# Kernel optimization log

Hardware: AMD Instinct MI355X
Metric: run time of the kernel (lower is better)

Reference implementation:

```python
import jax, jax.numpy as jnp
import numpy as np

DEPTH = 3
WIDTH = 512
WIDTH_SUB = 256
B = 64
L = 512
EPS = 1e-5
C_IN = 2 * WIDTH_SUB  # == WIDTH here, so per-depth params stack uniformly


def setup_inputs() -> dict:
    key = jax.random.key(0)
    ks = jax.random.split(key, 4)
    s = 1.0 / np.sqrt(C_IN).astype(np.float32)
    P_matrix = jax.random.normal(ks[0], (B, C_IN, L), jnp.float32)
    Wq = jax.random.normal(ks[1], (DEPTH, WIDTH, C_IN), jnp.float32) * s
    Wk = jax.random.normal(ks[2], (DEPTH, WIDTH, C_IN), jnp.float32) * s
    Wv = jax.random.normal(ks[3], (DEPTH, WIDTH, C_IN), jnp.float32) * s
    zeros = jnp.zeros((DEPTH, WIDTH), jnp.float32)
    ones = jnp.ones((DEPTH, WIDTH), jnp.float32)
    return {
        "P_matrix": P_matrix,
        "Wq": Wq, "bq": zeros, "gq": ones, "betaq": zeros,
        "Wk": Wk, "bk": zeros, "gk": ones, "betak": zeros,
        "Wv": Wv, "bv": zeros, "gv": ones, "betav": zeros,
    }


def _ncl_linear(x, W, b, gamma, beta):
    # x: [B, C, L]; Linear over channel dim, then BatchNorm1d (training stats) + ReLU
    y = jnp.einsum('bcl,oc->bol', x, W) + b[None, :, None]  # [B, O, L]
    mean = y.mean(axis=(0, 2), keepdims=True)
    var = y.var(axis=(0, 2), keepdims=True)  # biased, as torch BN uses for normalization
    y = (y - mean) * jax.lax.rsqrt(var + EPS) * gamma[None, :, None] + beta[None, :, None]
    return jax.nn.relu(y)


def reference(P_matrix, Wq, bq, gq, betaq, Wk, bk, gk, betak, Wv, bv, gv, betav):
    x = P_matrix
    for i in range(DEPTH):
        Q = _ncl_linear(x, Wq[i], bq[i], gq[i], betaq[i])  # [B, W, L]
        K = _ncl_linear(x, Wk[i], bk[i], gk[i], betak[i])
        V = _ncl_linear(x, Wv[i], bv[i], gv[i], betav[i])
        w = jnp.einsum('bcl,bdl->bcd', Q, K)  # [B, W, W], unscaled
        # nn.Softmax() with dim=None on a 3D tensor -> dim=0 in torch
        a = jax.nn.softmax(w, axis=0)
        x = jnp.einsum('bcd,bdl->bcl', a, V)  # [B, W, L]
    return x
```

## Files before the change

### kernel.cpp

```cpp
#include <hip/hip_runtime.h>
#include <hip/hip_fp8.h>
#include <stdint.h>

typedef __bf16 bf16_t;
typedef bf16_t bf16x8 __attribute__((ext_vector_type(8)));
typedef bf16_t bf16x4 __attribute__((ext_vector_type(4)));
typedef float  f32x4  __attribute__((ext_vector_type(4)));

#define MFMA_BF16(a,b,c) __builtin_amdgcn_mfma_f32_16x16x32_bf16(a,b,c,0,0,0)

__device__ __forceinline__ void load_lds16(const bf16_t* g, bf16_t* l) {
  __builtin_amdgcn_global_load_lds((const __attribute__((address_space(1))) void*)g,
                                   (__attribute__((address_space(3))) void*)l,
                                   16, 0, 0);
}

__device__ __forceinline__ float fp8_to_f(uint8_t b) {
  return (float)__builtin_bit_cast(__hip_fp8_e4m3, b);
}
__device__ __forceinline__ uint8_t f_to_fp8(float f) {
  return __builtin_bit_cast(uint8_t, __hip_fp8_e4m3(f));
}
__device__ __forceinline__ uint8_t fp8s_enc(float r) { return f_to_fp8(r * 256.f); }
__device__ __forceinline__ float   fp8s_dec(uint8_t b) { return fp8_to_f(b) * (1.f/256.f); }

__device__ __forceinline__ bf16x8 dec8(uint64_t v) {
  bf16x8 o;
#pragma unroll
  for (int j = 0; j < 8; ++j) o[j] = (bf16_t)fp8s_dec((uint8_t)(v >> (8*j)));
  return o;
}

__global__ __launch_bounds__(256) void cast_w_kern(const float* __restrict__ wq,
    const float* __restrict__ wk, const float* __restrict__ wv,
    bf16_t* __restrict__ whi, bf16_t* __restrict__ wlo) {
  const int i = blockIdx.x * 256 + threadIdx.x;
  const int idx = i * 4;
  const int p = idx / 786432;
  const int r = idx - p * 786432;
  const float* s = (p == 0 ? wq : (p == 1 ? wk : wv));
  float4 v = *(const float4*)(s + r);
  float f[4] = {v.x, v.y, v.z, v.w};
  bf16x4 hi, lo;
#pragma unroll
  for (int j = 0; j < 4; ++j) {
    bf16_t h = (bf16_t)f[j];
    hi[j] = h;
    lo[j] = (bf16_t)(f[j] - (float)h);
  }
  const size_t o = (size_t)p * 786432 + r;
  *(bf16x4*)(whi + o) = hi;
  *(bf16x4*)(wlo + o) = lo;
}

__global__ __launch_bounds__(256) void transpose_split_in_kern(
    const float* __restrict__ P, bf16_t* __restrict__ xh, uint8_t* __restrict__ xl) {
  __shared__ float t[32][33];
  const int bz = blockIdx.x >> 8;
  const int ti = blockIdx.x & 255;
  const int tc = (ti >> 4) * 32;
  const int tl = (ti & 15) * 32;
  const float* Pb = P + (size_t)bz * 262144;
  bf16_t* xb = xh + (size_t)bz * 262144;
  uint8_t* lb = xl + (size_t)bz * 262144;
  const int tx = threadIdx.x & 31, ty = threadIdx.x >> 5;
#pragma unroll
  for (int k = 0; k < 4; ++k)
    t[ty*4+k][tx] = Pb[(size_t)(tc + ty*4 + k)*512 + tl + tx];
  __syncthreads();
#pragma unroll
  for (int k = 0; k < 4; ++k) {
    const float f = t[tx][ty*4+k];
    const bf16_t h = (bf16_t)f;
    const size_t o = (size_t)(tl + ty*4 + k)*512 + tc + tx;
    xb[o] = h;
    lb[o] = fp8s_enc(f - (float)h);
  }
}

__global__ __launch_bounds__(256) void gemm_qkv_kern(
    const bf16_t* __restrict__ Whi, const bf16_t* __restrict__ Wlo,
    const bf16_t* __restrict__ xh, const uint8_t* __restrict__ xl,
    const float* __restrict__ bq, const float* __restrict__ bk,
    const float* __restrict__ bv, int depth,
    bf16_t* __restrict__ Qh, uint8_t* __restrict__ Ql,
    bf16_t* __restrict__ Kh, uint8_t* __restrict__ Kl,
    bf16_t* __restrict__ Yvh, bf16_t* __restrict__ Yvl,
    float* __restrict__ bsum, float* __restrict__ bsum2) {
  __shared__ __align__(16) bf16_t Ah[4096], Al[4096], Bh[4096], Bl[4096];
  const int blk = blockIdx.x;
  const int t  = blk & 15;
  const int pb = blk >> 4;
  const int b  = pb & 63, p = pb >> 6;
  const int row0 = (t >> 2) * 128, col0 = (t & 3) * 128;
  const size_t woff = (size_t)p * 786432 + (size_t)depth * 262144;
  const bf16_t* A_hi = Whi + woff;
  const bf16_t* A_lo = Wlo + woff;
  const bf16_t* B_hi = xh + (size_t)b * 262144;
  const uint8_t* B_lo = xl + (size_t)b * 262144;
  const int tid = threadIdx.x, lane = tid & 63, wid = tid >> 6;
  const int wm = wid >> 1, wn = wid & 1;
  const int sr = tid >> 2, scs = (tid & 3) * 8;
  const int frow = lane & 15, fk = (lane >> 4) * 8;
  f32x4 acc[4][4] = {};
  bf16_t* lah = Ah + wid * 512;
  bf16_t* lal = Al + wid * 512;
  bf16_t* lbh = Bh + wid * 512;
  const bf16_t* gah = A_hi + (size_t)(row0 + sr) * 512 + scs;
  const bf16_t* gal = A_lo + (size_t)(row0 + sr) * 512 + scs;
  const bf16_t* gbh = B_hi + (size_t)(col0 + sr) * 512 + scs;
  const uint8_t* gbl = B_lo + (size_t)(col0 + sr) * 512 + scs;
  for (int ks = 0; ks < 16; ++ks) {
    const int k0 = ks * 32;
    load_lds16(gah + k0, lah); load_lds16(gah + 32768 + k0, lah + 2048);
    load_lds16(gal + k0, lal); load_lds16(gal + 32768 + k0, lal + 2048);
    load_lds16(gbh + k0, lbh); load_lds16(gbh + 32768 + k0, lbh + 2048);
    {
      const uint64_t r0 = *(const uint64_t*)(gbl + k0);
      const uint64_t r1 = *(const uint64_t*)(gbl + 32768 + k0);
      *(bf16x8*)(Bl + sr*32 + scs)        = dec8(r0);
      *(bf16x8*)(Bl + 2048 + sr*32 + scs) = dec8(r1);
    }
    __syncthreads();
    bf16x8 ah[4], al[4], bh[4], bl[4];
#pragma unroll
    for (int i = 0; i < 4; ++i) {
      const int ai = (wm*64 + i*16 + frow)*32 + fk;
      const int bi = (wn*64 + i*16 + frow)*32 + fk;
      ah[i] = *(const bf16x8*)(Ah + ai);
      al[i] = *(const bf16x8*)(Al + ai);
      bh[i] = *(const bf16x8*)(Bh + bi);
      bl[i] = *(const bf16x8*)(Bl + bi);
    }
#pragma unroll
    for (int i = 0; i < 4; ++i)
#pragma unroll
      for (int j = 0; j < 4; ++j) {
        acc[i][j] = MFMA_BF16(ah[i], bh[j], acc[i][j]);
        acc[i][j] = MFMA_BF16(al[i], bh[j], acc[i][j]);
        acc[i][j] = MFMA_BF16(ah[i], bl[j], acc[i][j]);
      }
    __syncthreads();
  }
  const float* bias = (p == 0 ? bq : (p == 1 ? bk : bv)) + depth * 512;
  if (p < 2) {
    bf16_t* Oh = (p == 0 ? Qh : Kh) + (size_t)b * 262144;
    uint8_t* Ol = (p == 0 ? Ql : Kl) + (size_t)b * 262144;
#pragma unroll
    for (int i = 0; i < 4; ++i)
#pragma unroll
      for (int r = 0; r < 4; ++r) {
        const int rr = row0 + wm*64 + i*16 + (lane >> 4)*4 + r;
        const float bb = bias[rr];
        float s = 0.f, ss = 0.f;
#pragma unroll
        for (int j = 0; j < 4; ++j) {
          const int cc = col0 + wn*64 + j*16 + (lane & 15);
          const float y = acc[i][j][r] + bb;
          s += y; ss += y * y;
          const bf16_t h = (bf16_t)y;
          Oh[(size_t)rr * 512 + cc] = h;
          Ol[(size_t)rr * 512 + cc] = fp8s_enc(y - (float)h);
        }
#pragma unroll
        for (int m = 1; m < 16; m <<= 1) {
          s  += __shfl_xor(s, m);
          ss += __shfl_xor(ss, m);
        }
        if ((lane & 15) == 0) {
          atomicAdd(&bsum[p * 512 + rr], s);
          atomicAdd(&bsum2[p * 512 + rr], ss);
        }
      }
  } else {
    bf16_t* Ovh = Yvh + (size_t)b * 262144;
    bf16_t* Ovl = Yvl + (size_t)b * 262144;
#pragma unroll
    for (int i = 0; i < 4; ++i)
#pragma unroll
      for (int r = 0; r < 4; ++r) {
        const int rr = row0 + wm*64 + i*16 + (lane >> 4)*4 + r;
        const float bb = bias[rr];
        float s = 0.f, ss = 0.f;
#pragma unroll
        for (int j = 0; j < 4; ++j) {
          const int cc = col0 + wn*64 + j*16 + (lane & 15);
          const float y = acc[i][j][r] + bb;
          s += y; ss += y * y;
          const bf16_t h = (bf16_t)y;
          Ovh[(size_t)rr * 512 + cc] = h;
          Ovl[(size_t)rr * 512 + cc] = (bf16_t)(y - (float)h);
        }
#pragma unroll
        for (int m = 1; m < 16; m <<= 1) {
          s  += __shfl_xor(s, m);
          ss += __shfl_xor(ss, m);
        }
        if ((lane & 15) == 0) {
          atomicAdd(&bsum[1024 + rr], s);
          atomicAdd(&bsum2[1024 + rr], ss);
        }
      }
  }
}

__global__ __launch_bounds__(256) void bn_finalize_kern(
    float* __restrict__ bsum, float* __restrict__ bsum2,
    const float* __restrict__ gq, const float* __restrict__ gk, const float* __restrict__ gv,
    const float* __restrict__ betaq, const float* __restrict__ betak, const float* __restrict__ betav,
    int depth, float* __restrict__ scale, float* __restrict__ shift) {
  const int po = blockIdx.x * 256 + threadIdx.x;
  const int p = po >> 9, o = po & 511;
  const float mean = bsum[po] * (1.f / 32768.f);
  float var = bsum2[po] * (1.f / 32768.f) - mean * mean;
  var = fmaxf(var, 0.f);
  const float* gp = (p == 0 ? gq : (p == 1 ? gk : gv));
  const float* bp = (p == 0 ? betaq : (p == 1 ? betak : betav));
  const float gamma = gp[depth * 512 + o];
  const float beta  = bp[depth * 512 + o];
  const float sc = gamma * rsqrtf(var + 1e-5f);
  scale[po] = sc;
  shift[po] = beta - mean * sc;
  bsum[po] = 0.f;
  bsum2[po] = 0.f;
}

__global__ __launch_bounds__(256) void norm_qk_kern(
    bf16_t* __restrict__ Qh, uint8_t* __restrict__ Ql,
    bf16_t* __restrict__ Kh, uint8_t* __restrict__ Kl,
    const float* __restrict__ scale, const float* __restrict__ shift) {
  const size_t i = ((size_t)blockIdx.x * 256 + threadIdx.x) * 4;
  const int p = (int)(i >> 24);
  const size_t j = i & 0xFFFFFF;
  const int o = (int)(j >> 9) & 511;
  const int po = p * 512 + o;
  const float sc = scale[po], sh = shift[po];
  bf16_t* H = (p == 0 ? Qh : Kh) + j;
  uint8_t* L = (p == 0 ? Ql : Kl) + j;
  bf16x4 hv = *(bf16x4*)H;
  uint32_t lv = *(uint32_t*)L;
  bf16x4 ho;
  uint32_t lo_out = 0;
#pragma unroll
  for (int k = 0; k < 4; ++k) {
    const float y = (float)hv[k] + fp8s_dec((uint8_t)(lv >> (8*k)));
    const float q = fmaxf(y * sc + sh, 0.f);
    const bf16_t h = (bf16_t)q;
    ho[k] = h;
    lo_out |= (uint32_t)fp8s_enc(q - (float)h) << (8*k);
  }
  *(bf16x4*)H = ho;
  *(uint32_t*)L = lo_out;
}

__global__ __launch_bounds__(256) void norm_v_t_kern(
    const bf16_t* __restrict__ Yvh, const bf16_t* __restrict__ Yvl,
    const float* __restrict__ scale, const float* __restrict__ shift,
    bf16_t* __restrict__ VTh, uint8_t* __restrict__ VTl) {
  __shared__ float t[32][33];
  const int bz = blockIdx.x >> 8;
  const int ti = blockIdx.x & 255;
  const int td = (ti >> 4) * 32;
  const int tl = (ti & 15) * 32;
  const size_t boff = (size_t)bz * 262144;
  const int tx = threadIdx.x & 31, ty = threadIdx.x >> 5;
#pragma unroll
  for (int k = 0; k < 4; ++k) {
    const int dd = td + ty*4 + k;
    const float sc = scale[1024 + dd], sh = shift[1024 + dd];
    const size_t o = boff + (size_t)dd * 512 + tl + tx;
    const float f = (float)Yvh[o] + (float)Yvl[o];
    t[ty*4+k][tx] = fmaxf(f * sc + sh, 0.f);
  }
  __syncthreads();
#pragma unroll
  for (int k = 0; k < 4; ++k) {
    const float v = t[tx][ty*4+k];
    const bf16_t h = (bf16_t)v;
    const size_t o = boff + (size_t)(tl + ty*4 + k)*512 + td + tx;
    VTh[o] = h;
    VTl[o] = fp8s_enc(v - (float)h);
  }
}

__global__ __launch_bounds__(256) void gemm_w_kern(
    const bf16_t* __restrict__ Qh, const uint8_t* __restrict__ Ql,
    const bf16_t* __restrict__ Kh, const uint8_t* __restrict__ Kl,
    float* __restrict__ w) {
  __shared__ __align__(16) bf16_t Ah[4096], Al[4096], Bh[4096], Bl[4096];
  const int blk = blockIdx.x;
  const int t = blk & 15;
  const int b = blk >> 4;
  const int row0 = (t >> 2) * 128, col0 = (t & 3) * 128;
  const bf16_t* A_hi = Qh + (size_t)b * 262144;
  const uint8_t* A_lo = Ql + (size_t)b * 262144;
  const bf16_t* B_hi = Kh + (size_t)b * 262144;
  const uint8_t* B_lo = Kl + (size_t)b * 262144;
  const int tid = threadIdx.x, lane = tid & 63, wid = tid >> 6;
  const int wm = wid >> 1, wn = wid & 1;
  const int sr = tid >> 2, scs = (tid & 3) * 8;
  const int frow = lane & 15, fk = (lane >> 4) * 8;
  f32x4 acc[4][4] = {};
  bf16_t* lah = Ah + wid * 512;
  bf16_t* lbh = Bh + wid * 512;
  const bf16_t* gah = A_hi + (size_t)(row0 + sr) * 512 + scs;
  const bf16_t* gbh = B_hi + (size_t)(col0 + sr) * 512 + scs;
  const uint8_t* gal = A_lo + (size_t)(row0 + sr) * 512 + scs;
  const uint8_t* gbl = B_lo + (size_t)(col0 + sr) * 512 + scs;
  for (int ks = 0; ks < 16; ++ks) {
    const int k0 = ks * 32;
    load_lds16(gah + k0, lah); load_lds16(gah + 32768 + k0, lah + 2048);
    load_lds16(gbh + k0, lbh); load_lds16(gbh + 32768 + k0, lbh + 2048);
    {
      const uint64_t ra0 = *(const uint64_t*)(gal + k0);
      const uint64_t ra1 = *(const uint64_t*)(gal + 32768 + k0);
      const uint64_t rb0 = *(const uint64_t*)(gbl + k0);
      const uint64_t rb1 = *(const uint64_t*)(gbl + 32768 + k0);
      *(bf16x8*)(Al + sr*32 + scs)        = dec8(ra0);
      *(bf16x8*)(Al + 2048 + sr*32 + scs) = dec8(ra1);
      *(bf16x8*)(Bl + sr*32 + scs)        = dec8(rb0);
      *(bf16x8*)(Bl + 2048 + sr*32 + scs) = dec8(rb1);
    }
    __syncthreads();
    bf16x8 ah[4], al[4], bh[4], bl[4];
#pragma unroll
    for (int i = 0; i < 4; ++i) {
      const int ai = (wm*64 + i*16 + frow)*32 + fk;
      const int bi = (wn*64 + i*16 + frow)*32 + fk;
      ah[i] = *(const bf16x8*)(Ah + ai);
      al[i] = *(const bf16x8*)(Al + ai);
      bh[i] = *(const bf16x8*)(Bh + bi);
      bl[i] = *(const bf16x8*)(Bl + bi);
    }
#pragma unroll
    for (int i = 0; i < 4; ++i)
#pragma unroll
      for (int j = 0; j < 4; ++j) {
        acc[i][j] = MFMA_BF16(ah[i], bh[j], acc[i][j]);
        acc[i][j] = MFMA_BF16(al[i], bh[j], acc[i][j]);
        acc[i][j] = MFMA_BF16(ah[i], bl[j], acc[i][j]);
      }
    __syncthreads();
  }
  float* wb = w + (size_t)b * 262144;
#pragma unroll
  for (int i = 0; i < 4; ++i)
#pragma unroll
    for (int j = 0; j < 4; ++j)
#pragma unroll
      for (int r = 0; r < 4; ++r) {
        const int rr = row0 + wm*64 + i*16 + (lane >> 4)*4 + r;
        const int cc = col0 + wn*64 + j*16 + (lane & 15);
        wb[(size_t)rr * 512 + cc] = acc[i][j][r];
      }
}

__global__ __launch_bounds__(256) void softmax_kern(float* __restrict__ w) {
  const int idx = blockIdx.x * 256 + threadIdx.x;
  float v[64];
#pragma unroll
  for (int b = 0; b < 64; ++b) v[b] = w[idx + (size_t)b * 262144];
  float m = v[0];
#pragma unroll
  for (int b = 1; b < 64; ++b) m = fmaxf(m, v[b]);
  float s = 0.f;
#pragma unroll
  for (int b = 0; b < 64; ++b) { v[b] = __expf(v[b] - m); s += v[b]; }
  const float inv = 1.f / s;
#pragma unroll
  for (int b = 0; b < 64; ++b) w[idx + (size_t)b * 262144] = v[b] * inv;
}

__global__ __launch_bounds__(256) void gemm_x_kern(
    const bf16_t* __restrict__ VTh, const uint8_t* __restrict__ VTl,
    const float* __restrict__ a,
    bf16_t* __restrict__ xh, uint8_t* __restrict__ xl) {
  __shared__ __align__(16) bf16_t Ah[4096], Al[4096], Bh[4096], Bl[4096];
  const int blk = blockIdx.x;
  const int t = blk & 15;
  const int b = blk >> 4;
  const int row0 = (t >> 2) * 128, col0 = (t & 3) * 128;
  const bf16_t* Ahg = VTh + (size_t)b * 262144;
  const uint8_t* Alg = VTl + (size_t)b * 262144;
  const float*   Bg  = a   + (size_t)b * 262144;
  const int tid = threadIdx.x, lane = tid & 63, wid = tid >> 6;
  const int wm = wid >> 1, wn = wid & 1;
  const int sr = tid >> 2, scs = (tid & 3) * 8;
  const int frow = lane & 15, fk = (lane >> 4) * 8;
  f32x4 acc[4][4] = {};
  bf16_t* lah = Ah + wid * 512;
  const bf16_t* gah = Ahg + (size_t)(row0 + sr) * 512 + scs;
  const uint8_t* gal = Alg + (size_t)(row0 + sr) * 512 + scs;
  for (int ks = 0; ks < 16; ++ks) {
    const int k0 = ks * 32;
    load_lds16(gah + k0, lah); load_lds16(gah + 32768 + k0, lah + 2048);
    {
      const uint64_t r0 = *(const uint64_t*)(gal + k0);
      const uint64_t r1 = *(const uint64_t*)(gal + 32768 + k0);
      *(bf16x8*)(Al + sr*32 + scs)        = dec8(r0);
      *(bf16x8*)(Al + 2048 + sr*32 + scs) = dec8(r1);
    }
    {
#pragma unroll
      for (int p = 0; p < 4; ++p) {
        const int idx = p * 256 + tid;
        const int br = idx >> 3;
        const int cs = (idx & 7) * 4;
        float4 v4 = *(const float4*)(Bg + (size_t)(col0 + br) * 512 + k0 + cs);
        float f[4] = {v4.x, v4.y, v4.z, v4.w};
        bf16x4 hv, lv;
#pragma unroll
        for (int j = 0; j < 4; ++j) {
          bf16_t h = (bf16_t)f[j];
          hv[j] = h;
          lv[j] = (bf16_t)(f[j] - (float)h);
        }
        *(bf16x4*)(Bh + br*32 + cs) = hv;
        *(bf16x4*)(Bl + br*32 + cs) = lv;
      }
    }
    __syncthreads();
    bf16x8 ah[4], al[4], bh[4], bl[4];
#pragma unroll
    for (int i = 0; i < 4; ++i) {
      const int ai = (wm*64 + i*16 + frow)*32 + fk;
      const int bi = (wn*64 + i*16 + frow)*32 + fk;
      ah[i] = *(const bf16x8*)(Ah + ai);
      al[i] = *(const bf16x8*)(Al + ai);
      bh[i] = *(const bf16x8*)(Bh + bi);
      bl[i] = *(const bf16x8*)(Bl + bi);
    }
#pragma unroll
    for (int i = 0; i < 4; ++i)
#pragma unroll
      for (int j = 0; j < 4; ++j) {
        acc[i][j] = MFMA_BF16(ah[i], bh[j], acc[i][j]);
        acc[i][j] = MFMA_BF16(al[i], bh[j], acc[i][j]);
        acc[i][j] = MFMA_BF16(ah[i], bl[j], acc[i][j]);
      }
    __syncthreads();
  }
  bf16_t* xb = xh + (size_t)b * 262144;
  uint8_t* lb8 = xl + (size_t)b * 262144;
#pragma unroll
  for (int i = 0; i < 4; ++i)
#pragma unroll
    for (int j = 0; j < 4; ++j)
#pragma unroll
      for (int r = 0; r < 4; ++r) {
        const int rr = row0 + wm*64 + i*16 + (lane >> 4)*4 + r;
        const int cc = col0 + wn*64 + j*16 + (lane & 15);
        const float y = acc[i][j][r];
        const bf16_t h = (bf16_t)y;
        xb[(size_t)rr * 512 + cc] = h;
        lb8[(size_t)rr * 512 + cc] = fp8s_enc(y - (float)h);
      }
}

__global__ __launch_bounds__(256) void out_transpose_kern(
    const bf16_t* __restrict__ xh, const uint8_t* __restrict__ xl,
    float* __restrict__ out) {
  __shared__ float t[32][33];
  const int bz = blockIdx.x >> 8;
  const int ti = blockIdx.x & 255;
  const int tl = (ti >> 4) * 32;
  const int tc = (ti & 15) * 32;
  const bf16_t* xb = xh + (size_t)bz * 262144;
  const uint8_t* lb = xl + (size_t)bz * 262144;
  float* ob = out + (size_t)bz * 262144;
  const int tx = threadIdx.x & 31, ty = threadIdx.x >> 5;
#pragma unroll
  for (int k = 0; k < 4; ++k) {
    const size_t o = (size_t)(tl + ty*4 + k)*512 + tc + tx;
    t[ty*4+k][tx] = (float)xb[o] + fp8s_dec(lb[o]);
  }
  __syncthreads();
#pragma unroll
  for (int k = 0; k < 4; ++k)
    ob[(size_t)(tc + ty*4 + k)*512 + tl + tx] = t[tx][ty*4+k];
}

extern "C" void kernel_launch(void* const* d_in, const int* in_sizes, int n_in,
                              void* d_out, int out_size, void* d_ws, size_t ws_size,
                              hipStream_t stream) {
  const float* P     = (const float*)d_in[0];
  const float* Wq    = (const float*)d_in[1];
  const float* bq    = (const float*)d_in[2];
  const float* gq    = (const float*)d_in[3];
  const float* betaq = (const float*)d_in[4];
  const float* Wk    = (const float*)d_in[5];
  const float* bk    = (const float*)d_in[6];
  const float* gk    = (const float*)d_in[7];
  const float* betak = (const float*)d_in[8];
  const float* Wv    = (const float*)d_in[9];
  const float* bv    = (const float*)d_in[10];
  const float* gv    = (const float*)d_in[11];
  const float* betav = (const float*)d_in[12];

  char* ws = (char*)d_ws;
  size_t off = 0;
  auto alloc = [&](size_t bytes) -> char* {
    char* p = ws + off;
    off += (bytes + 255) & ~(size_t)255;
    return p;
  };
  bf16_t*  Sh[3]; uint8_t* Sl[3];
  for (int i = 0; i < 3; ++i) {
    Sh[i] = (bf16_t*) alloc(33554432);
    Sl[i] = (uint8_t*)alloc(16777216);
  }
  char* E = alloc(67108864);
  float*  w   = (float*)E;
  bf16_t* Yvh = (bf16_t*)E;
  bf16_t* Yvl = (bf16_t*)(E + 33554432);
  bf16_t* Whi = (bf16_t*)alloc(4718592);
  bf16_t* Wlo = (bf16_t*)alloc(4718592);
  float* scale = (float*)alloc(6144);
  float* shift = (float*)alloc(6144);
  float* bsum  = (float*)alloc(6144);
  float* bsum2 = (float*)alloc(6144);

  hipMemsetAsync(bsum, 0, 12288, stream);
  cast_w_kern<<<2304, 256, 0, stream>>>(Wq, Wk, Wv, Whi, Wlo);
  transpose_split_in_kern<<<16384, 256, 0, stream>>>(P, Sh[0], Sl[0]);
  for (int d = 0; d < 3; ++d) {
    const int xi = (d == 1) ? 1 : 0;
    const int qi = (d == 1) ? 0 : 1;
    const int ki = 2;
    const int ni = (d == 2) ? 2 : qi;
    gemm_qkv_kern<<<3072, 256, 0, stream>>>(Whi, Wlo, Sh[xi], Sl[xi],
        bq, bk, bv, d, Sh[qi], Sl[qi], Sh[ki], Sl[ki], Yvh, Yvl, bsum, bsum2);
    bn_finalize_kern<<<6, 256, 0, stream>>>(bsum, bsum2, gq, gk, gv,
        betaq, betak, betav, d, scale, shift);
    norm_qk_kern<<<32768, 256, 0, stream>>>(Sh[qi], Sl[qi], Sh[ki], Sl[ki],
        scale, shift);
    norm_v_t_kern<<<16384, 256, 0, stream>>>(Yvh, Yvl, scale, shift,
        Sh[xi], Sl[xi]);
    gemm_w_kern<<<1024, 256, 0, stream>>>(Sh[qi], Sl[qi], Sh[ki], Sl[ki], w);
    softmax_kern<<<1024, 256, 0, stream>>>(w);
    gemm_x_kern<<<1024, 256, 0, stream>>>(Sh[xi], Sl[xi], w, Sh[ni], Sl[ni]);
  }
  out_transpose_kern<<<16384, 256, 0, stream>>>(Sh[2], Sl[2], (float*)d_out);
}
```

Measured before the change: 1.718 ms.

## Swizzle LDS tiles in GEMMs and replace BN atomics with partial-sum buffer

Applies an XOR swizzle to the 16-byte column chunks of the LDS tiles in all three GEMM kernels, both on the write side (global source offsets / store positions) and on the fragment reads. The intent is to remove LDS bank conflicts on the MFMA operand loads. It also replaces the per-row atomicAdd accumulation of BatchNorm sums with a deterministic partial-statistics buffer that bn_finalize reduces with one wave per channel. This drops the atomics and the memset, at the cost of a larger scratch buffer and a wider finalize launch.

```diff
diff --git a/kernel.cpp b/kernel.cpp
--- a/kernel.cpp
+++ b/kernel.cpp
@@ -30,6 +30,7 @@
   for (int j = 0; j < 8; ++j) o[j] = (bf16_t)fp8s_dec((uint8_t)(v >> (8*j)));
   return o;
 }
+
 
 __global__ __launch_bounds__(256) void cast_w_kern(const float* __restrict__ wq,
     const float* __restrict__ wk, const float* __restrict__ wv,
@@ -86,13 +87,13 @@
     bf16_t* __restrict__ Qh, uint8_t* __restrict__ Ql,
     bf16_t* __restrict__ Kh, uint8_t* __restrict__ Kl,
     bf16_t* __restrict__ Yvh, bf16_t* __restrict__ Yvl,
-    float* __restrict__ bsum, float* __restrict__ bsum2) {
+    float2* __restrict__ pst) {
   __shared__ __align__(16) bf16_t Ah[4096], Al[4096], Bh[4096], Bl[4096];
   const int blk = blockIdx.x;
   const int t  = blk & 15;
   const int pb = blk >> 4;
   const int b  = pb & 63, p = pb >> 6;
-  const int row0 = (t >> 2) * 128, col0 = (t & 3) * 128;
+  const int row0 = (t >> 2) * 128, col0 = (t & 3) * 128, ct = t & 3;
   const size_t woff = (size_t)p * 786432 + (size_t)depth * 262144;
   const bf16_t* A_hi = Whi + woff;
   const bf16_t* A_lo = Wlo + woff;
@@ -100,16 +101,19 @@
   const uint8_t* B_lo = xl + (size_t)b * 262144;
   const int tid = threadIdx.x, lane = tid & 63, wid = tid >> 6;
   const int wm = wid >> 1, wn = wid & 1;
-  const int sr = tid >> 2, scs = (tid & 3) * 8;
-  const int frow = lane & 15, fk = (lane >> 4) * 8;
+  const int sr = tid >> 2;
+  const int scs    = (tid & 3) * 8;
+  const int scs_sw = (((tid & 3) ^ ((sr >> 1) & 3)) * 8);
+  const int frow = lane & 15;
+  const int fks = (((lane >> 4) ^ ((frow >> 1) & 3)) * 8);
   f32x4 acc[4][4] = {};
   bf16_t* lah = Ah + wid * 512;
   bf16_t* lal = Al + wid * 512;
   bf16_t* lbh = Bh + wid * 512;
-  const bf16_t* gah = A_hi + (size_t)(row0 + sr) * 512 + scs;
-  const bf16_t* gal = A_lo + (size_t)(row0 + sr) * 512 + scs;
-  const bf16_t* gbh = B_hi + (size_t)(col0 + sr) * 512 + scs;
-  const uint8_t* gbl = B_lo + (size_t)(col0 + sr) * 512 + scs;
+  const bf16_t* gah = A_hi + (size_t)(row0 + sr) * 512 + scs_sw;
+  const bf16_t* gal = A_lo + (size_t)(row0 + sr) * 512 + scs_sw;
+  const bf16_t* gbh = B_hi + (size_t)(col0 + sr) * 512 + scs_sw;
+  const uint8_t* gbl = B_lo + (size_t)(col0 + sr) * 512 + scs_sw;
   for (int ks = 0; ks < 16; ++ks) {
     const int k0 = ks * 32;
     load_lds16(gah + k0, lah); load_lds16(gah + 32768 + k0, lah + 2048);
@@ -125,8 +129,8 @@
     bf16x8 ah[4], al[4], bh[4], bl[4];
 #pragma unroll
     for (int i = 0; i < 4; ++i) {
-      const int ai = (wm*64 + i*16 + frow)*32 + fk;
-      const int bi = (wn*64 + i*16 + frow)*32 + fk;
+      const int ai = (wm*64 + i*16 + frow)*32 + fks;
+      const int bi = (wn*64 + i*16 + frow)*32 + fks;
       ah[i] = *(const bf16x8*)(Ah + ai);
       al[i] = *(const bf16x8*)(Al + ai);
       bh[i] = *(const bf16x8*)(Bh + bi);
@@ -143,6 +147,7 @@
     __syncthreads();
   }
   const float* bias = (p == 0 ? bq : (p == 1 ? bk : bv)) + depth * 512;
+  const int pi = b * 8 + ct * 2 + wn;
   if (p < 2) {
     bf16_t* Oh = (p == 0 ? Qh : Kh) + (size_t)b * 262144;
     uint8_t* Ol = (p == 0 ? Ql : Kl) + (size_t)b * 262144;
@@ -167,10 +172,8 @@
           s  += __shfl_xor(s, m);
           ss += __shfl_xor(ss, m);
         }
-        if ((lane & 15) == 0) {
-          atomicAdd(&bsum[p * 512 + rr], s);
-          atomicAdd(&bsum2[p * 512 + rr], ss);
-        }
+        if ((lane & 15) == 0)
+          pst[((size_t)(p * 512 + rr) << 9) + pi] = make_float2(s, ss);
       }
   } else {
     bf16_t* Ovh = Yvh + (size_t)b * 262144;
@@ -196,33 +199,41 @@
           s  += __shfl_xor(s, m);
           ss += __shfl_xor(ss, m);
         }
-        if ((lane & 15) == 0) {
-          atomicAdd(&bsum[1024 + rr], s);
-          atomicAdd(&bsum2[1024 + rr], ss);
-        }
+        if ((lane & 15) == 0)
+          pst[((size_t)(1024 + rr) << 9) + pi] = make_float2(s, ss);
       }
   }
 }
 
 __global__ __launch_bounds__(256) void bn_finalize_kern(
-    float* __restrict__ bsum, float* __restrict__ bsum2,
+    const float2* __restrict__ pst,
     const float* __restrict__ gq, const float* __restrict__ gk, const float* __restrict__ gv,
     const float* __restrict__ betaq, const float* __restrict__ betak, const float* __restrict__ betav,
     int depth, float* __restrict__ scale, float* __restrict__ shift) {
-  const int po = blockIdx.x * 256 + threadIdx.x;
-  const int p = po >> 9, o = po & 511;
-  const float mean = bsum[po] * (1.f / 32768.f);
-  float var = bsum2[po] * (1.f / 32768.f) - mean * mean;
-  var = fmaxf(var, 0.f);
-  const float* gp = (p == 0 ? gq : (p == 1 ? gk : gv));
-  const float* bp = (p == 0 ? betaq : (p == 1 ? betak : betav));
-  const float gamma = gp[depth * 512 + o];
-  const float beta  = bp[depth * 512 + o];
-  const float sc = gamma * rsqrtf(var + 1e-5f);
-  scale[po] = sc;
-  shift[po] = beta - mean * sc;
-  bsum[po] = 0.f;
-  bsum2[po] = 0.f;
+  const int lane = threadIdx.x & 63, w = threadIdx.x >> 6;
+  const int po = blockIdx.x * 4 + w;
+  const float2* src = pst + ((size_t)po << 9) + lane * 8;
+  float s = 0.f, ss = 0.f;
+#pragma unroll
+  for (int j = 0; j < 8; ++j) { s += src[j].x; ss += src[j].y; }
+#pragma unroll
+  for (int off = 32; off > 0; off >>= 1) {
+    s  += __shfl_down(s, off);
+    ss += __shfl_down(ss, off);
+  }
+  if (lane == 0) {
+    const int p = po >> 9, o = po & 511;
+    const float mean = s * (1.f / 32768.f);
+    float var = ss * (1.f / 32768.f) - mean * mean;
+    var = fmaxf(var, 0.f);
+    const float* gp = (p == 0 ? gq : (p == 1 ? gk : gv));
+    const float* bp = (p == 0 ? betaq : (p == 1 ? betak : betav));
+    const float gamma = gp[depth * 512 + o];
+    const float beta  = bp[depth * 512 + o];
+    const float sc = gamma * rsqrtf(var + 1e-5f);
+    scale[po] = sc;
+    shift[po] = beta - mean * sc;
+  }
 }
 
 __global__ __launch_bounds__(256) void norm_qk_kern(
@@ -298,15 +309,18 @@
   const uint8_t* B_lo = Kl + (size_t)b * 262144;
   const int tid = threadIdx.x, lane = tid & 63, wid = tid >> 6;
   const int wm = wid >> 1, wn = wid & 1;
-  const int sr = tid >> 2, scs = (tid & 3) * 8;
-  const int frow = lane & 15, fk = (lane >> 4) * 8;
+  const int sr = tid >> 2;
+  const int scs    = (tid & 3) * 8;
+  const int scs_sw = (((tid & 3) ^ ((sr >> 1) & 3)) * 8);
+  const int frow = lane & 15;
+  const int fks = (((lane >> 4) ^ ((frow >> 1) & 3)) * 8);
   f32x4 acc[4][4] = {};
   bf16_t* lah = Ah + wid * 512;
   bf16_t* lbh = Bh + wid * 512;
-  const bf16_t* gah = A_hi + (size_t)(row0 + sr) * 512 + scs;
-  const bf16_t* gbh = B_hi + (size_t)(col0 + sr) * 512 + scs;
-  const uint8_t* gal = A_lo + (size_t)(row0 + sr) * 512 + scs;
-  const uint8_t* gbl = B_lo + (size_t)(col0 + sr) * 512 + scs;
+  const bf16_t* gah = A_hi + (size_t)(row0 + sr) * 512 + scs_sw;
+  const bf16_t* gbh = B_hi + (size_t)(col0 + sr) * 512 + scs_sw;
+  const uint8_t* gal = A_lo + (size_t)(row0 + sr) * 512 + scs_sw;
+  const uint8_t* gbl = B_lo + (size_t)(col0 + sr) * 512 + scs_sw;
   for (int ks = 0; ks < 16; ++ks) {
     const int k0 = ks * 32;
     load_lds16(gah + k0, lah); load_lds16(gah + 32768 + k0, lah + 2048);
@@ -325,8 +339,8 @@
     bf16x8 ah[4], al[4], bh[4], bl[4];
 #pragma unroll
     for (int i = 0; i < 4; ++i) {
-      const int ai = (wm*64 + i*16 + frow)*32 + fk;
-      const int bi = (wn*64 + i*16 + frow)*32 + fk;
+      const int ai = (wm*64 + i*16 + frow)*32 + fks;
+      const int bi = (wn*64 + i*16 + frow)*32 + fks;
       ah[i] = *(const bf16x8*)(Ah + ai);
       al[i] = *(const bf16x8*)(Al + ai);
       bh[i] = *(const bf16x8*)(Bh + bi);
@@ -385,12 +399,15 @@
   const float*   Bg  = a   + (size_t)b * 262144;
   const int tid = threadIdx.x, lane = tid & 63, wid = tid >> 6;
   const int wm = wid >> 1, wn = wid & 1;
-  const int sr = tid >> 2, scs = (tid & 3) * 8;
-  const int frow = lane & 15, fk = (lane >> 4) * 8;
+  const int sr = tid >> 2;
+  const int scs    = (tid & 3) * 8;
+  const int scs_sw = (((tid & 3) ^ ((sr >> 1) & 3)) * 8);
+  const int frow = lane & 15;
+  const int fks = (((lane >> 4) ^ ((frow >> 1) & 3)) * 8);
   f32x4 acc[4][4] = {};
   bf16_t* lah = Ah + wid * 512;
-  const bf16_t* gah = Ahg + (size_t)(row0 + sr) * 512 + scs;
-  const uint8_t* gal = Alg + (size_t)(row0 + sr) * 512 + scs;
+  const bf16_t* gah = Ahg + (size_t)(row0 + sr) * 512 + scs_sw;
+  const uint8_t* gal = Alg + (size_t)(row0 + sr) * 512 + scs_sw;
   for (int ks = 0; ks < 16; ++ks) {
     const int k0 = ks * 32;
     load_lds16(gah + k0, lah); load_lds16(gah + 32768 + k0, lah + 2048);
@@ -406,6 +423,7 @@
         const int idx = p * 256 + tid;
         const int br = idx >> 3;
         const int cs = (idx & 7) * 4;
+        const int ps = ((cs >> 3) ^ ((br >> 1) & 3)) * 8 + (cs & 7);
         float4 v4 = *(const float4*)(Bg + (size_t)(col0 + br) * 512 + k0 + cs);
         float f[4] = {v4.x, v4.y, v4.z, v4.w};
         bf16x4 hv, lv;
@@ -415,16 +433,16 @@
           hv[j] = h;
           lv[j] = (bf16_t)(f[j] - (float)h);
         }
-        *(bf16x4*)(Bh + br*32 + cs) = hv;
-        *(bf16x4*)(Bl + br*32 + cs) = lv;
+        *(bf16x4*)(Bh + br*32 + ps) = hv;
+        *(bf16x4*)(Bl + br*32 + ps) = lv;
       }
     }
     __syncthreads();
     bf16x8 ah[4], al[4], bh[4], bl[4];
 #pragma unroll
     for (int i = 0; i < 4; ++i) {
-      const int ai = (wm*64 + i*16 + frow)*32 + fk;
-      const int bi = (wn*64 + i*16 + frow)*32 + fk;
+      const int ai = (wm*64 + i*16 + frow)*32 + fks;
+      const int bi = (wn*64 + i*16 + frow)*32 + fks;
       ah[i] = *(const bf16x8*)(Ah + ai);
       al[i] = *(const bf16x8*)(Al + ai);
       bh[i] = *(const bf16x8*)(Bh + bi);
@@ -517,10 +535,8 @@
   bf16_t* Wlo = (bf16_t*)alloc(4718592);
   float* scale = (float*)alloc(6144);
   float* shift = (float*)alloc(6144);
-  float* bsum  = (float*)alloc(6144);
-  float* bsum2 = (float*)alloc(6144);
-
-  hipMemsetAsync(bsum, 0, 12288, stream);
+  float2* pst = (float2*)alloc(6291456);
+
   cast_w_kern<<<2304, 256, 0, stream>>>(Wq, Wk, Wv, Whi, Wlo);
   transpose_split_in_kern<<<16384, 256, 0, stream>>>(P, Sh[0], Sl[0]);
   for (int d = 0; d < 3; ++d) {
@@ -529,8 +545,8 @@
     const int ki = 2;
     const int ni = (d == 2) ? 2 : qi;
     gemm_qkv_kern<<<3072, 256, 0, stream>>>(Whi, Wlo, Sh[xi], Sl[xi],
-        bq, bk, bv, d, Sh[qi], Sl[qi], Sh[ki], Sl[ki], Yvh, Yvl, bsum, bsum2);
-    bn_finalize_kern<<<6, 256, 0, stream>>>(bsum, bsum2, gq, gk, gv,
+        bq, bk, bv, d, Sh[qi], Sl[qi], Sh[ki], Sl[ki], Yvh, Yvl, pst);
+    bn_finalize_kern<<<384, 256, 0, stream>>>(pst, gq, gk, gv,
         betaq, betak, betav, d, scale, shift);
     norm_qk_kern<<<32768, 256, 0, stream>>>(Sh[qi], Sl[qi], Sh[ki], Sl[ki],
         scale, shift);
```

Result: faster. 1.508 ms (-12.2%).
